# Optimization experiments

Hardware: AMD Instinct MI355X
Metric: run time of the kernel (lower is better)

The kernel has to match this reference:

```python
import jax, jax.numpy as jnp
import numpy as np

B, N, D = 8, 8192, 512
HID_ATT = D // 8          # input_dim // num_heads = 64
TOPK = max(1, int(N * 0.3))  # 2457


def _mlp2(x, W1, b1, W2, b2):
    # 2-layer MLP: Linear -> GELU -> Linear (inference mode: dropout/norm off)
    h = jax.nn.gelu(x @ W1 + b1)
    return h @ W2 + b2


def setup_inputs() -> dict:
    key = jax.random.key(0)
    ks = jax.random.split(key, 9)
    s = lambda k, sh, fan: jax.random.normal(k, sh, jnp.float32) * (1.0 / np.sqrt(fan))
    return {
        "x": jax.random.normal(ks[0], (B, N, D), jnp.float32),
        # attention-score MLP: D -> HID_ATT -> 1
        "aW1": s(ks[1], (D, HID_ATT), D),
        "ab1": jnp.zeros((HID_ATT,), jnp.float32),
        "aW2": s(ks[2], (HID_ATT, 1), HID_ATT),
        "ab2": jnp.zeros((1,), jnp.float32),
        # projection MLP: D -> D -> D
        "pW1": s(ks[3], (D, D), D),
        "pb1": jnp.zeros((D,), jnp.float32),
        "pW2": s(ks[4], (D, D), D),
        "pb2": jnp.zeros((D,), jnp.float32),
    }


def reference(x, aW1, ab1, aW2, ab2, pW1, pb1, pW2, pb2):
    # per-instance attention score -> sigmoid weight, [B, N]
    weights = jax.nn.sigmoid(_mlp2(x, aW1, ab1, aW2, ab2)[..., 0])
    # top-k per bag (largest)
    topk_scores, topk_idx = jax.lax.top_k(weights, TOPK)  # [B, TOPK]
    # gather selected instances, scale by score, mean over selected -> [B, D]
    sel = jnp.take_along_axis(x, topk_idx[..., None], axis=1)  # [B, TOPK, D]
    emb = jnp.mean(sel * topk_scores[..., None], axis=1)       # [B, D]
    projection = _mlp2(emb, pW1, pb1, pW2, pb2)                # [B, D]
    return projection, weights
```

## Files before the change

kernel.cpp:

```cpp
#include <hip/hip_runtime.h>
#include <math.h>

#define B_BAGS 8
#define N_INST 8192
#define D_DIM  512
#define H_ATT  64
#define TOPK_K 2457
#define ROWS_TOTAL (B_BAGS * N_INST)

typedef __attribute__((ext_vector_type(8))) short bf16x8;
typedef __attribute__((ext_vector_type(4))) float f32x4;

#define WS_W1P_HI 0
#define WS_W1P_LO 65536
#define WS_PART3  131584
#define WS_PART1  (WS_PART3 + 8*64*512*4)
#define WS_THRESH (WS_PART1 + 16*8*512*4)

__device__ __forceinline__ unsigned short bf16_rn(float f) {
  unsigned int x = __float_as_uint(f);
  unsigned int r = (x + 0x7FFFu + ((x >> 16) & 1u)) >> 16;
  return (unsigned short)r;
}
__device__ __forceinline__ float bf16_f(unsigned short u) {
  return __uint_as_float(((unsigned int)u) << 16);
}
__device__ __forceinline__ float gelu_f(float v) {
  float u = 0.7978845608028654f * (v + 0.044715f * v * v * v);
  return 0.5f * v * (1.0f + tanhf(u));
}

__device__ __forceinline__ void cvt_hilo(const float4 u, const float4 v,
                                         bf16x8& h, bf16x8& l) {
  float f[8] = {u.x, u.y, u.z, u.w, v.x, v.y, v.z, v.w};
#pragma unroll
  for (int i = 0; i < 8; i++) {
    unsigned int b = __float_as_uint(f[i]);
    unsigned int hb = b & 0xFFFF0000u;
    float r = f[i] - __uint_as_float(hb);
    h[i] = (short)(b >> 16);
    l[i] = (short)(__float_as_uint(r) >> 16);
  }
}

__device__ __forceinline__ void load_lds16(const void* g, void* l) {
  __builtin_amdgcn_global_load_lds(
      (const __attribute__((address_space(1))) void*)g,
      (__attribute__((address_space(3))) void*)l, 16, 0, 0);
}

__global__ __launch_bounds__(256) void k_prep(const float* __restrict__ aW1,
                                              unsigned short* __restrict__ hi,
                                              unsigned short* __restrict__ lo) {
  int tau = blockIdx.x * 256 + threadIdx.x;
  if (tau >= 4096) return;
  int ks = tau >> 8, t = (tau >> 6) & 3, lane = tau & 63;
  int n = t * 16 + (lane & 15);
  int kb = ks * 32 + (lane >> 4) * 8;
#pragma unroll
  for (int j = 0; j < 8; j++) {
    float v = aW1[(kb + j) * H_ATT + n];
    unsigned short h = bf16_rn(v);
    unsigned short l = bf16_rn(v - bf16_f(h));
    hi[tau * 8 + j] = h;
    lo[tau * 8 + j] = l;
  }
}

#define BM 64
#define NCH 16
#define AUNIT2 1040
#define ABUF (8 * AUNIT2)

__global__ __launch_bounds__(256) void k_scores(
    const float* __restrict__ x,
    const unsigned short* __restrict__ w1p_hi,
    const unsigned short* __restrict__ w1p_lo,
    const float* __restrict__ ab1, const float* __restrict__ aW2,
    const float* __restrict__ ab2, float* __restrict__ wout) {
  __shared__ __align__(16) char Asm[2][ABUF];
  __shared__ __align__(16) char Bhs[2][4096];
  __shared__ __align__(16) char Bls[2][4096];

  int tid = threadIdx.x;
  int wave = tid >> 6, lane = tid & 63;
  int c0 = lane & 15, quad = lane >> 4;
  int rowBase0 = blockIdx.x * BM;

  f32x4 acc[4];
#pragma unroll
  for (int t = 0; t < 4; t++) acc[t] = (f32x4){0.f, 0.f, 0.f, 0.f};

  const int r = wave * 16 + c0;
  const int aoff = (r >> 3) * AUNIT2 + (r & 7) * 128 + quad * 32;

  auto stage = [&](int c, int pb) {
#pragma unroll
    for (int i = 0; i < 2; i++) {
      int u = wave * 2 + i;
      const char* g = (const char*)x +
          (size_t)(rowBase0 + u * 8 + (lane >> 3)) * 2048 +
          (size_t)c * 128 + (size_t)(lane & 7) * 16;
      load_lds16(g, &Asm[pb][u * AUNIT2]);
    }
    load_lds16((const char*)w1p_hi + (size_t)c * 4096 + wave * 1024 + lane * 16,
               &Bhs[pb][wave * 1024]);
    load_lds16((const char*)w1p_lo + (size_t)c * 4096 + wave * 1024 + lane * 16,
               &Bls[pb][wave * 1024]);
  };

  stage(0, 0);
  __syncthreads();

  for (int c = 0; c < NCH; c++) {
    int pb = c & 1;
    if (c + 1 < NCH) stage(c + 1, pb ^ 1);

    const float4 a0v = *reinterpret_cast<const float4*>(&Asm[pb][aoff]);
    const float4 a1v = *reinterpret_cast<const float4*>(&Asm[pb][aoff + 16]);
    bf16x8 afh, afl;
    cvt_hilo(a0v, a1v, afh, afl);
    bf16x8 bfh[4], bfl[4];
#pragma unroll
    for (int t = 0; t < 4; t++) {
      bfh[t] = *reinterpret_cast<const bf16x8*>(&Bhs[pb][t * 1024 + lane * 16]);
      bfl[t] = *reinterpret_cast<const bf16x8*>(&Bls[pb][t * 1024 + lane * 16]);
    }
#pragma unroll
    for (int t = 0; t < 4; t++) {
      acc[t] = __builtin_amdgcn_mfma_f32_16x16x32_bf16(afl, bfh[t], acc[t], 0, 0, 0);
      acc[t] = __builtin_amdgcn_mfma_f32_16x16x32_bf16(afh, bfl[t], acc[t], 0, 0, 0);
      acc[t] = __builtin_amdgcn_mfma_f32_16x16x32_bf16(afh, bfh[t], acc[t], 0, 0, 0);
    }
    __syncthreads();
  }

  float w2v[4], b1v[4];
#pragma unroll
  for (int t = 0; t < 4; t++) {
    w2v[t] = aW2[t * 16 + c0];
    b1v[t] = ab1[t * 16 + c0];
  }
  float bias2 = ab2[0];
  float p[4] = {0.f, 0.f, 0.f, 0.f};
#pragma unroll
  for (int t = 0; t < 4; t++)
#pragma unroll
    for (int rr = 0; rr < 4; rr++) {
      float h = gelu_f(acc[t][rr] + b1v[t]);
      p[rr] += h * w2v[t];
    }
#pragma unroll
  for (int off = 1; off < 16; off <<= 1)
#pragma unroll
    for (int rr = 0; rr < 4; rr++) p[rr] += __shfl_xor(p[rr], off, 64);
  if (c0 == 0) {
    int row = rowBase0 + wave * 16 + quad * 4;
#pragma unroll
    for (int rr = 0; rr < 4; rr++) {
      float sc = p[rr] + bias2;
      wout[row + rr] = 1.0f / (1.0f + expf(-sc));
    }
  }
}

__global__ __launch_bounds__(256) void k_thresh(const float* __restrict__ wout,
                                                unsigned int* __restrict__ thr) {
  int b = blockIdx.x;
  int tid = threadIdx.x;
  const float* w = wout + b * N_INST;

  unsigned int v[32];
#pragma unroll
  for (int j = 0; j < 32; j++) v[j] = __float_as_uint(w[j * 256 + tid]);

  __shared__ int red[2][4];
  int lane = tid & 63, wv = tid >> 6;
  int pb = 0;
  auto blocksum = [&](int c) -> int {
#pragma unroll
    for (int off = 32; off > 0; off >>= 1) c += __shfl_down(c, off, 64);
    if (lane == 0) red[pb][wv] = c;
    __syncthreads();
    int s = red[pb][0] + red[pb][1] + red[pb][2] + red[pb][3];
    pb ^= 1;
    return s;
  };

  unsigned int lo = 0u, hi = 0x3F800001u;
  while (hi - lo > 1u) {
    unsigned int mid = lo + ((hi - lo) >> 1);
    int c = 0;
#pragma unroll
    for (int j = 0; j < 32; j++) c += (v[j] >= mid) ? 1 : 0;
    if (blocksum(c) >= TOPK_K) lo = mid; else hi = mid;
  }
  unsigned int T = lo;
  int c1 = 0;
#pragma unroll
  for (int j = 0; j < 32; j++) c1 += (v[j] > T) ? 1 : 0;
  c1 = blocksum(c1);
  int needed = TOPK_K - c1;
  unsigned int tm = 0;
#pragma unroll
  for (int j = 0; j < 32; j++) tm |= (v[j] == T ? 1u : 0u) << j;
  int lom = -1, him = N_INST - 1;
  while (him - lom > 1) {
    int mid = (lom + him) >> 1;
    unsigned int mask = 0u;
    if (mid >= tid) {
      unsigned int jmax = (unsigned int)(mid - tid) >> 8;
      mask = (2u << jmax) - 1u;
    }
    if (blocksum((int)__popc(tm & mask)) >= needed) him = mid; else lom = mid;
  }
  if (tid == 0) {
    thr[b * 2] = T;
    thr[b * 2 + 1] = (unsigned int)him;
  }
}

__global__ __launch_bounds__(256) void k_gather(const float* __restrict__ x,
                                                const float* __restrict__ wout,
                                                const unsigned int* __restrict__ thr,
                                                float* __restrict__ part3) {
  int b = blockIdx.x >> 6;
  int blk = blockIdx.x & 63;
  int tid = threadIdx.x;
  const float* w = wout + b * N_INST;

  unsigned int T = thr[b * 2];
  int Icut = (int)thr[b * 2 + 1];

  __shared__ int idxs[128];
  __shared__ float wgts[128];
  __shared__ int wcnt[2];
  __shared__ float4 xfer[128];

  int lane = tid & 63;
  int r = blk * 128 + tid;
  bool sel = false;
  float wvv = 0.f;
  int pos = 0;
  if (tid < 128) {
    wvv = w[r];
    unsigned int wu = __float_as_uint(wvv);
    sel = (wu > T) || (wu == T && r <= Icut);
    unsigned long long m = __ballot(sel);
    pos = __popcll(m & ((1ull << lane) - 1ull));
    if (lane == 0) wcnt[tid >> 6] = __popcll(m);
  }
  __syncthreads();
  int total = wcnt[0] + wcnt[1];
  if (sel) {
    int base = (tid >= 64) ? wcnt[0] : 0;
    idxs[base + pos] = r;
    wgts[base + pos] = wvv;
  }
  __syncthreads();

  int half = tid >> 7;
  int L = tid & 127;
  float4 acc = {0.f, 0.f, 0.f, 0.f};
  const float* xb = x + (size_t)b * N_INST * D_DIM;
  int i2 = total & ~1;
#pragma unroll 4
  for (int i = 0; i < i2; i += 2) {
    int rr = idxs[i + half];
    float ww = wgts[i + half];
    const float4 xv = *reinterpret_cast<const float4*>(xb + (size_t)rr * D_DIM + L * 4);
    acc.x += ww * xv.x; acc.y += ww * xv.y; acc.z += ww * xv.z; acc.w += ww * xv.w;
  }
  if ((total & 1) && half == 0) {
    int rr = idxs[i2];
    float ww = wgts[i2];
    const float4 xv = *reinterpret_cast<const float4*>(xb + (size_t)rr * D_DIM + L * 4);
    acc.x += ww * xv.x; acc.y += ww * xv.y; acc.z += ww * xv.z; acc.w += ww * xv.w;
  }
  if (half == 1) xfer[L] = acc;
  __syncthreads();
  if (half == 0) {
    float4 o = xfer[L];
    acc.x += o.x; acc.y += o.y; acc.z += o.z; acc.w += o.w;
    *reinterpret_cast<float4*>(part3 + (size_t)(b * 64 + blk) * D_DIM + L * 4) = acc;
  }
}

__global__ __launch_bounds__(256) void k_proj1(const float* __restrict__ part3,
                                               const float* __restrict__ pW1,
                                               float* __restrict__ part1,
                                               const float* __restrict__ pb2,
                                               float* __restrict__ out) {
  int jt = blockIdx.x & 7, kt = blockIdx.x >> 3;
  __shared__ float emb_s[256];
  int tid = threadIdx.x;
  int col = tid & 63, bg = tid >> 6;
  if (kt == 0) {
    float bz = pb2[jt * 64 + col];
    out[(bg * 2) * 512 + jt * 64 + col] = bz;
    out[(bg * 2 + 1) * 512 + jt * 64 + col] = bz;
  }
  {
    int b = tid >> 5, d0 = tid & 31;
    const float* p = part3 + (size_t)b * 64 * 512 + kt * 32 + d0;
    float e = 0.f;
#pragma unroll 8
    for (int j = 0; j < 64; j++) e += p[j * 512];
    emb_s[b * 32 + d0] = e * (1.0f / TOPK_K);
  }
  __syncthreads();
  float a0 = 0.f, a1 = 0.f;
  const float* wrow = pW1 + (size_t)(kt * 32) * 512 + jt * 64 + col;
#pragma unroll 8
  for (int q = 0; q < 32; q++) {
    float wq = wrow[q * 512];
    a0 += emb_s[(bg * 2) * 32 + q] * wq;
    a1 += emb_s[(bg * 2 + 1) * 32 + q] * wq;
  }
  part1[kt * 4096 + (bg * 2) * 512 + jt * 64 + col] = a0;
  part1[kt * 4096 + (bg * 2 + 1) * 512 + jt * 64 + col] = a1;
}

__global__ __launch_bounds__(256) void k_proj2(const float* __restrict__ part1,
                                               const float* __restrict__ pb1,
                                               const float* __restrict__ pW2,
                                               float* __restrict__ out) {
  int jt = blockIdx.x & 7, kt = blockIdx.x >> 3;
  __shared__ float h_s[256];
  int tid = threadIdx.x;
  {
    int b = tid >> 5, j0 = tid & 31;
    int jj = kt * 32 + j0;
    float s = pb1[jj];
#pragma unroll
    for (int p = 0; p < 16; p++) s += part1[p * 4096 + b * 512 + jj];
    h_s[b * 32 + j0] = gelu_f(s);
  }
  __syncthreads();
  int col = tid & 63, bg = tid >> 6;
  float a0 = 0.f, a1 = 0.f;
  const float* wrow = pW2 + (size_t)(kt * 32) * 512 + jt * 64 + col;
#pragma unroll 8
  for (int q = 0; q < 32; q++) {
    float wq = wrow[q * 512];
    a0 += h_s[(bg * 2) * 32 + q] * wq;
    a1 += h_s[(bg * 2 + 1) * 32 + q] * wq;
  }
  atomicAdd(&out[(bg * 2) * 512 + jt * 64 + col], a0);
  atomicAdd(&out[(bg * 2 + 1) * 512 + jt * 64 + col], a1);
}

extern "C" void kernel_launch(void* const* d_in, const int* in_sizes, int n_in,
                              void* d_out, int out_size, void* d_ws, size_t ws_size,
                              hipStream_t stream) {
  (void)in_sizes; (void)n_in; (void)out_size; (void)ws_size;
  const float* x   = (const float*)d_in[0];
  const float* aW1 = (const float*)d_in[1];
  const float* ab1 = (const float*)d_in[2];
  const float* aW2 = (const float*)d_in[3];
  const float* ab2 = (const float*)d_in[4];
  const float* pW1 = (const float*)d_in[5];
  const float* pb1 = (const float*)d_in[6];
  const float* pW2 = (const float*)d_in[7];
  const float* pb2 = (const float*)d_in[8];

  float* out  = (float*)d_out;
  float* wout = out + B_BAGS * D_DIM;

  char* ws = (char*)d_ws;
  unsigned short* w1p_hi = (unsigned short*)(ws + WS_W1P_HI);
  unsigned short* w1p_lo = (unsigned short*)(ws + WS_W1P_LO);
  float* part3 = (float*)(ws + WS_PART3);
  float* part1 = (float*)(ws + WS_PART1);
  unsigned int* thr = (unsigned int*)(ws + WS_THRESH);

  k_prep<<<dim3(16), dim3(256), 0, stream>>>(aW1, w1p_hi, w1p_lo);
  k_scores<<<dim3(ROWS_TOTAL / BM), dim3(256), 0, stream>>>(x, w1p_hi, w1p_lo, ab1, aW2, ab2, wout);
  k_thresh<<<dim3(B_BAGS), dim3(256), 0, stream>>>(wout, thr);
  k_gather<<<dim3(B_BAGS * 64), dim3(256), 0, stream>>>(x, wout, thr, part3);
  k_proj1<<<dim3(128), dim3(256), 0, stream>>>(part3, pW1, part1, pb2, out);
  k_proj2<<<dim3(128), dim3(256), 0, stream>>>(part1, pb1, pW2, out);
}
```

Baseline: 256.4 us.

## Fuse gather with projection MLP via atomic accumulation and last-block reduction

Replaces per-block partial embedding writes with atomic accumulation into a per-bag embedding buffer. The last block of each bag, found with an atomic counter, then runs both projection layers itself. This removes two kernel launches and the partial-sum buffers. In exchange, the projection matvecs now run on only 8 blocks serially after the gather, and the float atomics make the summation order nondeterministic.

```diff
diff --git a/kernel.cpp b/kernel.cpp
--- a/kernel.cpp
+++ b/kernel.cpp
@@ -13,9 +13,9 @@
 
 #define WS_W1P_HI 0
 #define WS_W1P_LO 65536
-#define WS_PART3  131584
-#define WS_PART1  (WS_PART3 + 8*64*512*4)
-#define WS_THRESH (WS_PART1 + 16*8*512*4)
+#define WS_EMB    131584
+#define WS_CNT    (WS_EMB + 8*512*4)
+#define WS_THRESH (WS_CNT + 64)
 
 __device__ __forceinline__ unsigned short bf16_rn(float f) {
   unsigned int x = __float_as_uint(f);
@@ -51,9 +51,13 @@
 
 __global__ __launch_bounds__(256) void k_prep(const float* __restrict__ aW1,
                                               unsigned short* __restrict__ hi,
-                                              unsigned short* __restrict__ lo) {
+                                              unsigned short* __restrict__ lo,
+                                              float* __restrict__ emb_acc,
+                                              unsigned int* __restrict__ cnt) {
   int tau = blockIdx.x * 256 + threadIdx.x;
   if (tau >= 4096) return;
+  emb_acc[tau] = 0.f;
+  if (tau < 8) cnt[tau] = 0u;
   int ks = tau >> 8, t = (tau >> 6) & 3, lane = tau & 63;
   int n = t * 16 + (lane & 15);
   int kb = ks * 32 + (lane >> 4) * 8;
@@ -220,10 +224,13 @@
   }
 }
 
-__global__ __launch_bounds__(256) void k_gather(const float* __restrict__ x,
-                                                const float* __restrict__ wout,
-                                                const unsigned int* __restrict__ thr,
-                                                float* __restrict__ part3) {
+__global__ __launch_bounds__(256) void k_gatherproj(
+    const float* __restrict__ x, const float* __restrict__ wout,
+    const unsigned int* __restrict__ thr,
+    const float* __restrict__ pW1, const float* __restrict__ pb1,
+    const float* __restrict__ pW2, const float* __restrict__ pb2,
+    float* __restrict__ emb_acc, unsigned int* __restrict__ cnt,
+    float* __restrict__ out) {
   int b = blockIdx.x >> 6;
   int blk = blockIdx.x & 63;
   int tid = threadIdx.x;
@@ -236,6 +243,9 @@
   __shared__ float wgts[128];
   __shared__ int wcnt[2];
   __shared__ float4 xfer[128];
+  __shared__ float ebuf[512];
+  __shared__ float hbuf[512];
+  __shared__ int lastflag;
 
   int lane = tid & 63;
   int r = blk * 128 + tid;
@@ -282,72 +292,54 @@
   if (half == 0) {
     float4 o = xfer[L];
     acc.x += o.x; acc.y += o.y; acc.z += o.z; acc.w += o.w;
-    *reinterpret_cast<float4*>(part3 + (size_t)(b * 64 + blk) * D_DIM + L * 4) = acc;
-  }
-}
-
-__global__ __launch_bounds__(256) void k_proj1(const float* __restrict__ part3,
-                                               const float* __restrict__ pW1,
-                                               float* __restrict__ part1,
-                                               const float* __restrict__ pb2,
-                                               float* __restrict__ out) {
-  int jt = blockIdx.x & 7, kt = blockIdx.x >> 3;
-  __shared__ float emb_s[256];
-  int tid = threadIdx.x;
-  int col = tid & 63, bg = tid >> 6;
-  if (kt == 0) {
-    float bz = pb2[jt * 64 + col];
-    out[(bg * 2) * 512 + jt * 64 + col] = bz;
-    out[(bg * 2 + 1) * 512 + jt * 64 + col] = bz;
-  }
+    float* e = emb_acc + (size_t)b * D_DIM + L * 4;
+    atomicAdd(e + 0, acc.x);
+    atomicAdd(e + 1, acc.y);
+    atomicAdd(e + 2, acc.z);
+    atomicAdd(e + 3, acc.w);
+  }
+
+  __threadfence();
+  __syncthreads();
+  if (tid == 0) {
+    unsigned int old = atomicAdd(&cnt[b], 1u);
+    lastflag = (old == 63u) ? 1 : 0;
+  }
+  __syncthreads();
+  if (!lastflag) return;
+
+  __threadfence();
+  for (int k = tid; k < D_DIM; k += 256) {
+    float v = __hip_atomic_load(&emb_acc[(size_t)b * D_DIM + k],
+                                __ATOMIC_ACQUIRE, __HIP_MEMORY_SCOPE_AGENT);
+    ebuf[k] = v * (1.0f / TOPK_K);
+  }
+  __syncthreads();
   {
-    int b = tid >> 5, d0 = tid & 31;
-    const float* p = part3 + (size_t)b * 64 * 512 + kt * 32 + d0;
-    float e = 0.f;
+    int j0 = tid * 2;
+    float s0 = pb1[j0], s1 = pb1[j0 + 1];
 #pragma unroll 8
-    for (int j = 0; j < 64; j++) e += p[j * 512];
-    emb_s[b * 32 + d0] = e * (1.0f / TOPK_K);
-  }
-  __syncthreads();
-  float a0 = 0.f, a1 = 0.f;
-  const float* wrow = pW1 + (size_t)(kt * 32) * 512 + jt * 64 + col;
+    for (int k = 0; k < D_DIM; k++) {
+      float e = ebuf[k];
+      const float2 wv = *reinterpret_cast<const float2*>(&pW1[(size_t)k * D_DIM + j0]);
+      s0 += e * wv.x; s1 += e * wv.y;
+    }
+    hbuf[j0] = gelu_f(s0);
+    hbuf[j0 + 1] = gelu_f(s1);
+  }
+  __syncthreads();
+  {
+    int d0 = tid * 2;
+    float s0 = pb2[d0], s1 = pb2[d0 + 1];
 #pragma unroll 8
-  for (int q = 0; q < 32; q++) {
-    float wq = wrow[q * 512];
-    a0 += emb_s[(bg * 2) * 32 + q] * wq;
-    a1 += emb_s[(bg * 2 + 1) * 32 + q] * wq;
-  }
-  part1[kt * 4096 + (bg * 2) * 512 + jt * 64 + col] = a0;
-  part1[kt * 4096 + (bg * 2 + 1) * 512 + jt * 64 + col] = a1;
-}
-
-__global__ __launch_bounds__(256) void k_proj2(const float* __restrict__ part1,
-                                               const float* __restrict__ pb1,
-                                               const float* __restrict__ pW2,
-                                               float* __restrict__ out) {
-  int jt = blockIdx.x & 7, kt = blockIdx.x >> 3;
-  __shared__ float h_s[256];
-  int tid = threadIdx.x;
-  {
-    int b = tid >> 5, j0 = tid & 31;
-    int jj = kt * 32 + j0;
-    float s = pb1[jj];
-#pragma unroll
-    for (int p = 0; p < 16; p++) s += part1[p * 4096 + b * 512 + jj];
-    h_s[b * 32 + j0] = gelu_f(s);
-  }
-  __syncthreads();
-  int col = tid & 63, bg = tid >> 6;
-  float a0 = 0.f, a1 = 0.f;
-  const float* wrow = pW2 + (size_t)(kt * 32) * 512 + jt * 64 + col;
-#pragma unroll 8
-  for (int q = 0; q < 32; q++) {
-    float wq = wrow[q * 512];
-    a0 += h_s[(bg * 2) * 32 + q] * wq;
-    a1 += h_s[(bg * 2 + 1) * 32 + q] * wq;
-  }
-  atomicAdd(&out[(bg * 2) * 512 + jt * 64 + col], a0);
-  atomicAdd(&out[(bg * 2 + 1) * 512 + jt * 64 + col], a1);
+    for (int k = 0; k < D_DIM; k++) {
+      float h = hbuf[k];
+      const float2 wv = *reinterpret_cast<const float2*>(&pW2[(size_t)k * D_DIM + d0]);
+      s0 += h * wv.x; s1 += h * wv.y;
+    }
+    out[b * D_DIM + d0] = s0;
+    out[b * D_DIM + d0 + 1] = s1;
+  }
 }
 
 extern "C" void kernel_launch(void* const* d_in, const int* in_sizes, int n_in,
@@ -370,14 +362,13 @@
   char* ws = (char*)d_ws;
   unsigned short* w1p_hi = (unsigned short*)(ws + WS_W1P_HI);
   unsigned short* w1p_lo = (unsigned short*)(ws + WS_W1P_LO);
-  float* part3 = (float*)(ws + WS_PART3);
-  float* part1 = (float*)(ws + WS_PART1);
+  float* emb_acc = (float*)(ws + WS_EMB);
+  unsigned int* cnt = (unsigned int*)(ws + WS_CNT);
   unsigned int* thr = (unsigned int*)(ws + WS_THRESH);
 
-  k_prep<<<dim3(16), dim3(256), 0, stream>>>(aW1, w1p_hi, w1p_lo);
+  k_prep<<<dim3(16), dim3(256), 0, stream>>>(aW1, w1p_hi, w1p_lo, emb_acc, cnt);
   k_scores<<<dim3(ROWS_TOTAL / BM), dim3(256), 0, stream>>>(x, w1p_hi, w1p_lo, ab1, aW2, ab2, wout);
   k_thresh<<<dim3(B_BAGS), dim3(256), 0, stream>>>(wout, thr);
-  k_gather<<<dim3(B_BAGS * 64), dim3(256), 0, stream>>>(x, wout, thr, part3);
-  k_proj1<<<dim3(128), dim3(256), 0, stream>>>(part3, pW1, part1, pb2, out);
-  k_proj2<<<dim3(128), dim3(256), 0, stream>>>(part1, pb1, pW2, out);
-}
+  k_gatherproj<<<dim3(B_BAGS * 64), dim3(256), 0, stream>>>(
+      x, wout, thr, pW1, pb1, pW2, pb2, emb_acc, cnt, out);
+}
```

New measurement: 355.3 us. +38.6%, slower.

## Load x and packed W1 directly from global memory instead of LDS staging

Applied to the files above, without the earlier changes.

The score kernel no longer stages x tiles and the packed hi/lo W1 fragments through double-buffered shared memory with async global-to-LDS loads and per-chunk barriers. Each lane now reads its own 32 bytes of x and the weight fragments directly from global memory, with the loop unrolled by two. This removes the LDS traffic, the shared-memory footprint and the block synchronisation, but gives up explicit prefetch overlap. Each lane also reads only 32 bytes per 2 KB row per iteration, so coalescing is poor and the kernel depends on L2/cache for reuse.

```diff
diff --git a/kernel.cpp b/kernel.cpp
--- a/kernel.cpp
+++ b/kernel.cpp
@@ -41,12 +41,6 @@
     h[i] = (short)(b >> 16);
     l[i] = (short)(__float_as_uint(r) >> 16);
   }
-}
-
-__device__ __forceinline__ void load_lds16(const void* g, void* l) {
-  __builtin_amdgcn_global_load_lds(
-      (const __attribute__((address_space(1))) void*)g,
-      (__attribute__((address_space(3))) void*)l, 16, 0, 0);
 }
 
 __global__ __launch_bounds__(256) void k_prep(const float* __restrict__ aW1,
@@ -69,8 +63,6 @@
 
 #define BM 64
 #define NCH 16
-#define AUNIT2 1040
-#define ABUF (8 * AUNIT2)
 
 __global__ __launch_bounds__(256) void k_scores(
     const float* __restrict__ x,
@@ -78,53 +70,31 @@
     const unsigned short* __restrict__ w1p_lo,
     const float* __restrict__ ab1, const float* __restrict__ aW2,
     const float* __restrict__ ab2, float* __restrict__ wout) {
-  __shared__ __align__(16) char Asm[2][ABUF];
-  __shared__ __align__(16) char Bhs[2][4096];
-  __shared__ __align__(16) char Bls[2][4096];
-
   int tid = threadIdx.x;
   int wave = tid >> 6, lane = tid & 63;
   int c0 = lane & 15, quad = lane >> 4;
   int rowBase0 = blockIdx.x * BM;
 
+  const int row = rowBase0 + wave * 16 + c0;
+  const float* arow = x + (size_t)row * D_DIM;
+
   f32x4 acc[4];
 #pragma unroll
   for (int t = 0; t < 4; t++) acc[t] = (f32x4){0.f, 0.f, 0.f, 0.f};
 
-  const int r = wave * 16 + c0;
-  const int aoff = (r >> 3) * AUNIT2 + (r & 7) * 128 + quad * 32;
-
-  auto stage = [&](int c, int pb) {
-#pragma unroll
-    for (int i = 0; i < 2; i++) {
-      int u = wave * 2 + i;
-      const char* g = (const char*)x +
-          (size_t)(rowBase0 + u * 8 + (lane >> 3)) * 2048 +
-          (size_t)c * 128 + (size_t)(lane & 7) * 16;
-      load_lds16(g, &Asm[pb][u * AUNIT2]);
-    }
-    load_lds16((const char*)w1p_hi + (size_t)c * 4096 + wave * 1024 + lane * 16,
-               &Bhs[pb][wave * 1024]);
-    load_lds16((const char*)w1p_lo + (size_t)c * 4096 + wave * 1024 + lane * 16,
-               &Bls[pb][wave * 1024]);
-  };
-
-  stage(0, 0);
-  __syncthreads();
-
+#pragma unroll 2
   for (int c = 0; c < NCH; c++) {
-    int pb = c & 1;
-    if (c + 1 < NCH) stage(c + 1, pb ^ 1);
-
-    const float4 a0v = *reinterpret_cast<const float4*>(&Asm[pb][aoff]);
-    const float4 a1v = *reinterpret_cast<const float4*>(&Asm[pb][aoff + 16]);
+    const float* ap = arow + c * 32 + quad * 8;
+    const float4 a0v = *reinterpret_cast<const float4*>(ap);
+    const float4 a1v = *reinterpret_cast<const float4*>(ap + 4);
     bf16x8 afh, afl;
     cvt_hilo(a0v, a1v, afh, afl);
     bf16x8 bfh[4], bfl[4];
 #pragma unroll
     for (int t = 0; t < 4; t++) {
-      bfh[t] = *reinterpret_cast<const bf16x8*>(&Bhs[pb][t * 1024 + lane * 16]);
-      bfl[t] = *reinterpret_cast<const bf16x8*>(&Bls[pb][t * 1024 + lane * 16]);
+      size_t fo = ((size_t)(c * 4 + t) * 64 + lane) * 8;
+      bfh[t] = *reinterpret_cast<const bf16x8*>(w1p_hi + fo);
+      bfl[t] = *reinterpret_cast<const bf16x8*>(w1p_lo + fo);
     }
 #pragma unroll
     for (int t = 0; t < 4; t++) {
@@ -132,7 +102,6 @@
       acc[t] = __builtin_amdgcn_mfma_f32_16x16x32_bf16(afh, bfl[t], acc[t], 0, 0, 0);
       acc[t] = __builtin_amdgcn_mfma_f32_16x16x32_bf16(afh, bfh[t], acc[t], 0, 0, 0);
     }
-    __syncthreads();
   }
 
   float w2v[4], b1v[4];
@@ -155,11 +124,11 @@
 #pragma unroll
     for (int rr = 0; rr < 4; rr++) p[rr] += __shfl_xor(p[rr], off, 64);
   if (c0 == 0) {
-    int row = rowBase0 + wave * 16 + quad * 4;
+    int orow = rowBase0 + wave * 16 + quad * 4;
 #pragma unroll
     for (int rr = 0; rr < 4; rr++) {
       float sc = p[rr] + bias2;
-      wout[row + rr] = 1.0f / (1.0f + expf(-sc));
+      wout[orow + rr] = 1.0f / (1.0f + expf(-sc));
     }
   }
 }
```

After: 261.5 us. About the same (+2.0%).
